# Kernel optimization log

Hardware: AMD Instinct MI355X
Metric: run time of the kernel (lower is better)

Reference implementation:

```python
import jax, jax.numpy as jnp
import numpy as np

ALPHA = 0.2  # LeakyReLU negative slope
NEG_INF = -9e15


def setup_inputs() -> dict:
    key = jax.random.key(0)
    k1, k2, k3, k4 = jax.random.split(key, 4)
    B, C_in, N, L, F_out = 8, 32, 2048, 12, 32
    h = jax.random.normal(k1, (B, C_in, N, L), dtype=jnp.float32)
    adj = jax.random.randint(k2, (N, N), 0, 2, dtype=jnp.int32)
    # xavier_uniform with gain=1.414
    def xavier(k, shape, gain=1.414):
        fan_in, fan_out = shape[0], shape[1]
        bound = gain * np.sqrt(6.0 / (fan_in + fan_out))
        return jax.random.uniform(k, shape, jnp.float32, -bound, bound)
    W = xavier(k3, (C_in, F_out))
    a = xavier(k4, (2 * F_out, 1))
    return {"h": h, "adj": adj, "W": W, "a": a}


def reference(h, adj, W, a):
    # h: (B, C_in, N, L); W: (C_in, F); a: (2F, 1); adj: (N, N)
    B, C_in, N, L = h.shape
    F_out = W.shape[1]
    # Wh: (B, L, N, F)  == torch's (B*L, N, F) reshaped
    Wh = jnp.einsum('bcnl,cf->blnf', h, W)
    # Attention scores use only the last time step (torch slices [:, -1] of e)
    Wh_last = Wh[:, -1]                      # (B, N, F)
    s1 = Wh_last @ a[:F_out, 0]              # (B, N)
    s2 = Wh_last @ a[F_out:, 0]              # (B, N)
    e = s1[:, :, None] + s2[:, None, :]      # (B, N, N)
    e = jnp.where(e > 0, e, ALPHA * e)       # LeakyReLU
    e = jnp.where(adj[None] > 0, e, NEG_INF)
    attn = jax.nn.softmax(e, axis=1)         # softmax over rows (dim=1)
    # dropout skipped (eval mode)
    # h_prime[b,l,w,f] = sum_v Wh[b,l,v,f] * attn[b,v,w]
    h_prime = jnp.einsum('blvf,bvw->blwf', Wh, attn)
    out = jax.nn.elu(h_prime)                # concat=True branch
    return out.transpose(0, 3, 2, 1)         # (B, F, N, L)
```

## Files before the change

kernel.cpp:

```cpp
#include <hip/hip_runtime.h>
#include <hip/hip_bf16.h>
#include <math.h>


constexpr int Cin = 32;
constexpr int Nn  = 2048;
constexpr int Ln  = 12;
constexpr int Fn  = 32;
constexpr int LF  = Ln * Fn;
constexpr int NW  = Nn / 32;
constexpr int CH  = 128;
constexpr int NCH = Nn / CH;
constexpr int WT  = 64;
constexpr int MH  = 192;

typedef short short8 __attribute__((ext_vector_type(8)));
typedef float f32x4  __attribute__((ext_vector_type(4)));

static __device__ __forceinline__ unsigned short f2bf(float x) {
    unsigned u = __builtin_bit_cast(unsigned, x);
    u += 0x7FFFu + ((u >> 16) & 1u);
    return (unsigned short)(u >> 16);
}

__global__ __launch_bounds__(256) void k_adjbits(const int* __restrict__ adj,
                                                 unsigned* __restrict__ bits) {
    int id = blockIdx.x * 256 + threadIdx.x;
    int w  = id & (Nn - 1);
    int vw = id >> 11;
    unsigned m = 0u;
    int base = vw * 32 * Nn + w;
    #pragma unroll
    for (int k = 0; k < 32; ++k)
        m |= (adj[base + k * Nn] > 0 ? 1u : 0u) << k;
    bits[w * NW + vw] = m;
}

__global__ __launch_bounds__(256) void k_wh(const float* __restrict__ h,
                                            const float* __restrict__ W,
                                            const float* __restrict__ a,
                                            unsigned short* __restrict__ WhT,
                                            float* __restrict__ s1,
                                            float* __restrict__ s2,
                                            float* __restrict__ E1,
                                            float* __restrict__ E2) {
    __shared__ float hs[Cin][8][Ln];
    __shared__ float Ws[Cin][Fn];
    int b  = blockIdx.y;
    int n0 = blockIdx.x * 8;
    int tid = threadIdx.x;
    for (int i = tid; i < Cin * Fn; i += 256) Ws[i >> 5][i & 31] = W[i];
    for (int i = tid; i < Cin * 8 * Ln; i += 256) {
        int c = i / (8 * Ln);
        int r = i % (8 * Ln);
        hs[c][r / Ln][r % Ln] = h[(((size_t)b * Cin + c) * Nn + (n0 + r / Ln)) * Ln + (r % Ln)];
    }
    __syncthreads();
    int f  = tid & 31;
    int nl = tid >> 5;
    int n  = n0 + nl;
    float last = 0.f;
    #pragma unroll
    for (int l = 0; l < Ln; ++l) {
        float acc = 0.f;
        #pragma unroll
        for (int c = 0; c < Cin; ++c) acc += hs[c][nl][l] * Ws[c][f];
        WhT[((size_t)b * LF + l * Fn + f) * Nn + n] = f2bf(acc);
        if (l == Ln - 1) last = acc;
    }
    float r1 = last * a[f];
    float r2 = last * a[Fn + f];
    #pragma unroll
    for (int off = 16; off >= 1; off >>= 1) {
        r1 += __shfl_xor(r1, off);
        r2 += __shfl_xor(r2, off);
    }
    if (f == 0) {
        s1[b * Nn + n] = r1;
        s2[b * Nn + n] = r2;
        E1[b * Nn + n] = __expf(r1);
        E2[b * Nn + n] = __expf(0.2f * r1);
    }
}

__global__ __launch_bounds__(256) void k_smax(const float* __restrict__ s1,
                                              float* __restrict__ Mb) {
    int b = blockIdx.x;
    float m = -1e30f;
    for (int i = threadIdx.x; i < Nn; i += 256) m = fmaxf(m, s1[b * Nn + i]);
    #pragma unroll
    for (int off = 32; off >= 1; off >>= 1) m = fmaxf(m, __shfl_xor(m, off));
    __shared__ float wr[4];
    if ((threadIdx.x & 63) == 0) wr[threadIdx.x >> 6] = m;
    __syncthreads();
    if (threadIdx.x == 0)
        Mb[b] = fmaxf(fmaxf(wr[0], wr[1]), fmaxf(wr[2], wr[3]));
}

__global__ __launch_bounds__(256) void k_colinfo(const unsigned* __restrict__ bits,
                                                 int* __restrict__ empty) {
    int w = blockIdx.x * 256 + threadIdx.x;
    const uint4* p = (const uint4*)(bits + (size_t)w * NW);
    unsigned acc = 0;
    #pragma unroll
    for (int i = 0; i < 16; ++i) { uint4 v = p[i]; acc |= v.x | v.y | v.z | v.w; }
    empty[w] = (acc == 0u) ? 1 : 0;
}

__global__ __launch_bounds__(256, 2) void k_gemm(const unsigned short* __restrict__ WhT,
                                                 const float* __restrict__ s2,
                                                 const float* __restrict__ Mb,
                                                 const float* __restrict__ E1,
                                                 const float* __restrict__ E2,
                                                 const unsigned* __restrict__ bits,
                                                 const int* __restrict__ empty,
                                                 float* __restrict__ out) {
    int id = blockIdx.x;
    int b_ = id & 7;
    int r2 = id >> 3;
    int wt = r2 & 31;
    int mh = r2 >> 5;
    int w0 = wt * WT;
    int tid  = threadIdx.x;
    int lane = tid & 63;
    int wv   = tid >> 6;
    int lr   = lane & 15;
    int lg   = lane >> 4;
    int rbase = mh * MH + wv * 48;

    __shared__ unsigned short P[2][WT * CH];
    __shared__ float denom[WT];

    int vgrp = tid & 15;
    int wgrp = tid >> 4;
    int vs   = vgrp * 8;

    const float* E1b = E1 + (size_t)b_ * Nn;
    const float* E2b = E2 + (size_t)b_ * Nn;

    float F1[4], F2[4], G[4], Uv[4];
    float MbV = Mb[b_];
    #pragma unroll
    for (int i = 0; i < 4; ++i) {
        int w = w0 + wgrp * 4 + i;
        float s2w = s2[(size_t)b_ * Nn + w];
        float mz  = MbV + s2w;
        float mw  = fmaxf(mz, 0.2f * mz);
        F1[i] = __expf(s2w - mw);
        F2[i] = __expf(0.2f * s2w - mw);
        G[i]  = __expf(-s2w);
        Uv[i] = empty[w] ? 1.0f : 0.0f;
    }

    if (tid < WT) denom[tid] = 0.f;
    __syncthreads();

    auto gen = [&](int c, int buf) {
        int v0 = c * CH + vs;
        f32x4 e1a = *(const f32x4*)(E1b + v0);
        f32x4 e1b = *(const f32x4*)(E1b + v0 + 4);
        f32x4 e2a = *(const f32x4*)(E2b + v0);
        f32x4 e2b = *(const f32x4*)(E2b + v0 + 4);
        int wi = v0 >> 5;
        int sh = v0 & 31;
        float dsum[4];
        #pragma unroll
        for (int i = 0; i < 4; ++i) {
            int wl = wgrp * 4 + i;
            unsigned bm = (bits[(size_t)(w0 + wl) * NW + wi] >> sh) & 0xffu;
            short8 sv;
            float ds = 0.f;
            #pragma unroll
            for (int j = 0; j < 8; ++j) {
                float e1 = (j < 4) ? e1a[j] : e1b[j - 4];
                float e2 = (j < 4) ? e2a[j] : e2b[j - 4];
                bool pos = e1 > G[i];
                float t = (pos ? e1 : e2) * (pos ? F1[i] : F2[i]);
                float p = ((bm >> j) & 1u) ? t : Uv[i];
                ds += p;
                sv[j] = (short)f2bf(p);
            }
            int idx = (wl * CH + vs) ^ ((wl & 7) << 3);
            *(short8*)&P[buf][idx] = sv;
            dsum[i] = ds;
        }
        #pragma unroll
        for (int off = 1; off < 16; off <<= 1) {
            #pragma unroll
            for (int i = 0; i < 4; ++i) dsum[i] += __shfl_xor(dsum[i], off);
        }
        if (vgrp == 0) {
            #pragma unroll
            for (int i = 0; i < 4; ++i) denom[wgrp * 4 + i] += dsum[i];
        }
    };

    f32x4 acc[3][4];
    #pragma unroll
    for (int r = 0; r < 3; ++r)
        #pragma unroll
        for (int nf = 0; nf < 4; ++nf) acc[r][nf] = (f32x4){0.f, 0.f, 0.f, 0.f};

    const unsigned short* Ab = WhT + (size_t)b_ * LF * Nn;
    const unsigned short* Arow[3];
    #pragma unroll
    for (int r = 0; r < 3; ++r)
        Arow[r] = Ab + (size_t)(rbase + r * 16 + lr) * Nn;

    auto mfma_chunk = [&](int c, int buf) {
        #pragma unroll
        for (int ks = 0; ks < 4; ++ks) {
            int vb = c * CH + ks * 32 + lg * 8;
            short8 af[3];
            #pragma unroll
            for (int r = 0; r < 3; ++r)
                af[r] = *(const short8*)(Arow[r] + vb);
            #pragma unroll
            for (int nf = 0; nf < 4; ++nf) {
                int row = nf * 16 + lr;
                int idx = (row * CH + ks * 32 + lg * 8) ^ ((row & 7) << 3);
                short8 bf = *(const short8*)&P[buf][idx];
                #pragma unroll
                for (int r = 0; r < 3; ++r)
                    acc[r][nf] = __builtin_amdgcn_mfma_f32_16x16x32_bf16(af[r], bf, acc[r][nf], 0, 0, 0);
            }
        }
    };

    gen(0, 0);
    __syncthreads();
    for (int c = 0; c < NCH - 1; ++c) {
        gen(c + 1, (c + 1) & 1);
        mfma_chunk(c, c & 1);
        __syncthreads();
    }
    mfma_chunk(NCH - 1, (NCH - 1) & 1);

    float rdv[4];
    #pragma unroll
    for (int nf = 0; nf < 4; ++nf) rdv[nf] = 1.0f / denom[nf * 16 + lr];

    #pragma unroll
    for (int r = 0; r < 3; ++r)
        #pragma unroll
        for (int nf = 0; nf < 4; ++nf)
            #pragma unroll
            for (int q = 0; q < 4; ++q) {
                int lf = rbase + r * 16 + lg * 4 + q;
                int l = lf >> 5, f = lf & 31;
                float v = acc[r][nf][q] * rdv[nf];
                v = (v > 0.f) ? v : expm1f(v);
                out[(((size_t)b_ * Fn + f) * Nn + (w0 + nf * 16 + lr)) * Ln + l] = v;
            }
}

extern "C" void kernel_launch(void* const* d_in, const int* in_sizes, int n_in,
                              void* d_out, int out_size, void* d_ws, size_t ws_size,
                              hipStream_t stream) {
    (void)in_sizes; (void)n_in; (void)out_size; (void)ws_size;
    const float* h   = (const float*)d_in[0];
    const int*   adj = (const int*)d_in[1];
    const float* W   = (const float*)d_in[2];
    const float* a   = (const float*)d_in[3];
    float* out = (float*)d_out;

    char* ws = (char*)d_ws;
    unsigned short* WhT = (unsigned short*)(ws);
    float*    s1    = (float*)(ws + 12582912);
    float*    s2    = (float*)(ws + 12648448);
    float*    E1    = (float*)(ws + 12713984);
    float*    E2    = (float*)(ws + 12779520);
    float*    Mb    = (float*)(ws + 12845056);
    unsigned* bits  = (unsigned*)(ws + 12845312);
    int*      empty = (int*)(ws + 13369600);

    k_adjbits<<<512, 256, 0, stream>>>(adj, bits);
    k_wh<<<dim3(256, 8), 256, 0, stream>>>(h, W, a, WhT, s1, s2, E1, E2);
    k_smax<<<8, 256, 0, stream>>>(s1, Mb);
    k_colinfo<<<8, 256, 0, stream>>>(bits, empty);
    k_gemm<<<512, 256, 0, stream>>>(WhT, s2, Mb, E1, E2, bits, empty, out);
}
```

Baseline: 223.9 us.

## Restructure GEMM tiling, coalesce Wh and output stores, merge aux kernels

The attention GEMM now gives each block all 384 L·F rows for a 32-column tile, using 512 threads with one column per thread group. Probabilities for that tile are therefore generated once instead of twice across M halves. The epilogue stages accumulators through shared memory so each thread writes 12 contiguous floats with vector stores. k_wh transposes its bf16 results through shared memory for coalesced 16-byte stores and keeps W in registers. The two small reduction kernels are merged into one launch. The trade-offs are more LDS use and extra barriers per block.

```diff
diff --git a/kernel.cpp b/kernel.cpp
--- a/kernel.cpp
+++ b/kernel.cpp
@@ -3,7 +3,6 @@
 #include <math.h>
 
 
-constexpr int Cin = 32;
 constexpr int Nn  = 2048;
 constexpr int Ln  = 12;
 constexpr int Fn  = 32;
@@ -11,8 +10,7 @@
 constexpr int NW  = Nn / 32;
 constexpr int CH  = 128;
 constexpr int NCH = Nn / CH;
-constexpr int WT  = 64;
-constexpr int MH  = 192;
+constexpr int WT  = 32;
 
 typedef short short8 __attribute__((ext_vector_type(8)));
 typedef float f32x4  __attribute__((ext_vector_type(4)));
@@ -44,28 +42,37 @@
                                             float* __restrict__ s2,
                                             float* __restrict__ E1,
                                             float* __restrict__ E2) {
-    __shared__ float hs[Cin][8][Ln];
-    __shared__ float Ws[Cin][Fn];
+    __shared__ float hs[96][33];
+    __shared__ unsigned short T2[8][392];
     int b  = blockIdx.y;
     int n0 = blockIdx.x * 8;
     int tid = threadIdx.x;
-    for (int i = tid; i < Cin * Fn; i += 256) Ws[i >> 5][i & 31] = W[i];
-    for (int i = tid; i < Cin * 8 * Ln; i += 256) {
-        int c = i / (8 * Ln);
-        int r = i % (8 * Ln);
-        hs[c][r / Ln][r % Ln] = h[(((size_t)b * Cin + c) * Nn + (n0 + r / Ln)) * Ln + (r % Ln)];
-    }
-    __syncthreads();
+
+    for (int i = tid; i < 32 * 96; i += 256) {
+        int c = i / 96, r = i % 96;
+        hs[r][c] = h[(size_t)(b * 32 + c) * (Nn * Ln) + n0 * Ln + r];
+    }
     int f  = tid & 31;
     int nl = tid >> 5;
-    int n  = n0 + nl;
+    float Wc[32];
+    #pragma unroll
+    for (int c = 0; c < 32; ++c) Wc[c] = W[c * 32 + f];
+    __syncthreads();
+
     float last = 0.f;
     #pragma unroll
     for (int l = 0; l < Ln; ++l) {
+        const float* hr = &hs[nl * Ln + l][0];
         float acc = 0.f;
         #pragma unroll
-        for (int c = 0; c < Cin; ++c) acc += hs[c][nl][l] * Ws[c][f];
-        WhT[((size_t)b * LF + l * Fn + f) * Nn + n] = f2bf(acc);
+        for (int cq = 0; cq < 8; ++cq) {
+            f32x4 hv = *(const f32x4*)(hr + cq * 4);
+            acc = fmaf(hv[0], Wc[cq * 4 + 0], acc);
+            acc = fmaf(hv[1], Wc[cq * 4 + 1], acc);
+            acc = fmaf(hv[2], Wc[cq * 4 + 2], acc);
+            acc = fmaf(hv[3], Wc[cq * 4 + 3], acc);
+        }
+        T2[nl][l * 32 + f] = f2bf(acc);
         if (l == Ln - 1) last = acc;
     }
     float r1 = last * a[f];
@@ -76,38 +83,49 @@
         r2 += __shfl_xor(r2, off);
     }
     if (f == 0) {
+        int n = n0 + nl;
         s1[b * Nn + n] = r1;
         s2[b * Nn + n] = r2;
         E1[b * Nn + n] = __expf(r1);
         E2[b * Nn + n] = __expf(0.2f * r1);
     }
-}
-
-__global__ __launch_bounds__(256) void k_smax(const float* __restrict__ s1,
-                                              float* __restrict__ Mb) {
-    int b = blockIdx.x;
-    float m = -1e30f;
-    for (int i = threadIdx.x; i < Nn; i += 256) m = fmaxf(m, s1[b * Nn + i]);
-    #pragma unroll
-    for (int off = 32; off >= 1; off >>= 1) m = fmaxf(m, __shfl_xor(m, off));
-    __shared__ float wr[4];
-    if ((threadIdx.x & 63) == 0) wr[threadIdx.x >> 6] = m;
-    __syncthreads();
-    if (threadIdx.x == 0)
-        Mb[b] = fmaxf(fmaxf(wr[0], wr[1]), fmaxf(wr[2], wr[3]));
-}
-
-__global__ __launch_bounds__(256) void k_colinfo(const unsigned* __restrict__ bits,
-                                                 int* __restrict__ empty) {
-    int w = blockIdx.x * 256 + threadIdx.x;
-    const uint4* p = (const uint4*)(bits + (size_t)w * NW);
-    unsigned acc = 0;
-    #pragma unroll
-    for (int i = 0; i < 16; ++i) { uint4 v = p[i]; acc |= v.x | v.y | v.z | v.w; }
-    empty[w] = (acc == 0u) ? 1 : 0;
-}
-
-__global__ __launch_bounds__(256, 2) void k_gemm(const unsigned short* __restrict__ WhT,
+    __syncthreads();
+    for (int r = tid; r < LF; r += 256) {
+        unsigned d0 = (unsigned)T2[0][r] | ((unsigned)T2[1][r] << 16);
+        unsigned d1 = (unsigned)T2[2][r] | ((unsigned)T2[3][r] << 16);
+        unsigned d2 = (unsigned)T2[4][r] | ((unsigned)T2[5][r] << 16);
+        unsigned d3 = (unsigned)T2[6][r] | ((unsigned)T2[7][r] << 16);
+        uint4 val = {d0, d1, d2, d3};
+        *(uint4*)&WhT[((size_t)b * LF + r) * Nn + n0] = val;
+    }
+}
+
+__global__ __launch_bounds__(256) void k_aux(const float* __restrict__ s1,
+                                             const unsigned* __restrict__ bits,
+                                             float* __restrict__ Mb,
+                                             int* __restrict__ empty) {
+    if (blockIdx.x < 8) {
+        int b = blockIdx.x;
+        float m = -1e30f;
+        for (int i = threadIdx.x; i < Nn; i += 256) m = fmaxf(m, s1[b * Nn + i]);
+        #pragma unroll
+        for (int off = 32; off >= 1; off >>= 1) m = fmaxf(m, __shfl_xor(m, off));
+        __shared__ float wr[4];
+        if ((threadIdx.x & 63) == 0) wr[threadIdx.x >> 6] = m;
+        __syncthreads();
+        if (threadIdx.x == 0)
+            Mb[b] = fmaxf(fmaxf(wr[0], wr[1]), fmaxf(wr[2], wr[3]));
+    } else {
+        int w = (blockIdx.x - 8) * 256 + threadIdx.x;
+        const uint4* p = (const uint4*)(bits + (size_t)w * NW);
+        unsigned acc = 0;
+        #pragma unroll
+        for (int i = 0; i < 16; ++i) { uint4 v = p[i]; acc |= v.x | v.y | v.z | v.w; }
+        empty[w] = (acc == 0u) ? 1 : 0;
+    }
+}
+
+__global__ __launch_bounds__(512, 4) void k_gemm(const unsigned short* __restrict__ WhT,
                                                  const float* __restrict__ s2,
                                                  const float* __restrict__ Mb,
                                                  const float* __restrict__ E1,
@@ -117,89 +135,64 @@
                                                  float* __restrict__ out) {
     int id = blockIdx.x;
     int b_ = id & 7;
-    int r2 = id >> 3;
-    int wt = r2 & 31;
-    int mh = r2 >> 5;
+    int wt = id >> 3;
     int w0 = wt * WT;
     int tid  = threadIdx.x;
     int lane = tid & 63;
     int wv   = tid >> 6;
     int lr   = lane & 15;
     int lg   = lane >> 4;
-    int rbase = mh * MH + wv * 48;
+    int rbase = wv * 48;
 
     __shared__ unsigned short P[2][WT * CH];
+    __shared__ float T[LF][17];
     __shared__ float denom[WT];
 
     int vgrp = tid & 15;
-    int wgrp = tid >> 4;
+    int wl   = tid >> 4;
     int vs   = vgrp * 8;
+    int w    = w0 + wl;
 
     const float* E1b = E1 + (size_t)b_ * Nn;
     const float* E2b = E2 + (size_t)b_ * Nn;
-
-    float F1[4], F2[4], G[4], Uv[4];
-    float MbV = Mb[b_];
-    #pragma unroll
-    for (int i = 0; i < 4; ++i) {
-        int w = w0 + wgrp * 4 + i;
-        float s2w = s2[(size_t)b_ * Nn + w];
-        float mz  = MbV + s2w;
-        float mw  = fmaxf(mz, 0.2f * mz);
-        F1[i] = __expf(s2w - mw);
-        F2[i] = __expf(0.2f * s2w - mw);
-        G[i]  = __expf(-s2w);
-        Uv[i] = empty[w] ? 1.0f : 0.0f;
-    }
-
-    if (tid < WT) denom[tid] = 0.f;
-    __syncthreads();
+    const unsigned* bw = bits + (size_t)w * NW;
+
+    float s2w = s2[(size_t)b_ * Nn + w];
+    float mz  = Mb[b_] + s2w;
+    float mw  = fmaxf(mz, 0.2f * mz);
+    float F1  = __expf(s2w - mw);
+    float F2  = __expf(0.2f * s2w - mw);
+    float G   = __expf(-s2w);
+    float Uv  = empty[w] ? 1.0f : 0.0f;
+    float dsum = 0.f;
 
     auto gen = [&](int c, int buf) {
         int v0 = c * CH + vs;
         f32x4 e1a = *(const f32x4*)(E1b + v0);
-        f32x4 e1b = *(const f32x4*)(E1b + v0 + 4);
+        f32x4 e1c = *(const f32x4*)(E1b + v0 + 4);
         f32x4 e2a = *(const f32x4*)(E2b + v0);
-        f32x4 e2b = *(const f32x4*)(E2b + v0 + 4);
-        int wi = v0 >> 5;
-        int sh = v0 & 31;
-        float dsum[4];
-        #pragma unroll
-        for (int i = 0; i < 4; ++i) {
-            int wl = wgrp * 4 + i;
-            unsigned bm = (bits[(size_t)(w0 + wl) * NW + wi] >> sh) & 0xffu;
-            short8 sv;
-            float ds = 0.f;
-            #pragma unroll
-            for (int j = 0; j < 8; ++j) {
-                float e1 = (j < 4) ? e1a[j] : e1b[j - 4];
-                float e2 = (j < 4) ? e2a[j] : e2b[j - 4];
-                bool pos = e1 > G[i];
-                float t = (pos ? e1 : e2) * (pos ? F1[i] : F2[i]);
-                float p = ((bm >> j) & 1u) ? t : Uv[i];
-                ds += p;
-                sv[j] = (short)f2bf(p);
-            }
-            int idx = (wl * CH + vs) ^ ((wl & 7) << 3);
-            *(short8*)&P[buf][idx] = sv;
-            dsum[i] = ds;
-        }
-        #pragma unroll
-        for (int off = 1; off < 16; off <<= 1) {
-            #pragma unroll
-            for (int i = 0; i < 4; ++i) dsum[i] += __shfl_xor(dsum[i], off);
-        }
-        if (vgrp == 0) {
-            #pragma unroll
-            for (int i = 0; i < 4; ++i) denom[wgrp * 4 + i] += dsum[i];
-        }
+        f32x4 e2c = *(const f32x4*)(E2b + v0 + 4);
+        unsigned bm = (bw[v0 >> 5] >> (v0 & 31)) & 0xffu;
+        short8 sv;
+        #pragma unroll
+        for (int j = 0; j < 8; ++j) {
+            float e1 = (j < 4) ? e1a[j] : e1c[j - 4];
+            float e2 = (j < 4) ? e2a[j] : e2c[j - 4];
+            bool pos = e1 > G;
+            float t = (pos ? e1 : e2) * (pos ? F1 : F2);
+            float p = ((bm >> j) & 1u) ? t : Uv;
+            dsum += p;
+            sv[j] = (short)f2bf(p);
+        }
+        int idx = (wl * CH + vs) ^ ((wl & 7) << 3);
+        *(short8*)&P[buf][idx] = sv;
     };
 
-    f32x4 acc[3][4];
+    f32x4 acc[3][2];
     #pragma unroll
     for (int r = 0; r < 3; ++r)
         #pragma unroll
-        for (int nf = 0; nf < 4; ++nf) acc[r][nf] = (f32x4){0.f, 0.f, 0.f, 0.f};
+        for (int nf = 0; nf < 2; ++nf) acc[r][nf] = (f32x4){0.f, 0.f, 0.f, 0.f};
 
     const unsigned short* Ab = WhT + (size_t)b_ * LF * Nn;
     const unsigned short* Arow[3];
@@ -216,7 +209,7 @@
             for (int r = 0; r < 3; ++r)
                 af[r] = *(const short8*)(Arow[r] + vb);
             #pragma unroll
-            for (int nf = 0; nf < 4; ++nf) {
+            for (int nf = 0; nf < 2; ++nf) {
                 int row = nf * 16 + lr;
                 int idx = (row * CH + ks * 32 + lg * 8) ^ ((row & 7) << 3);
                 short8 bf = *(const short8*)&P[buf][idx];
@@ -236,22 +229,36 @@
     }
     mfma_chunk(NCH - 1, (NCH - 1) & 1);
 
-    float rdv[4];
-    #pragma unroll
-    for (int nf = 0; nf < 4; ++nf) rdv[nf] = 1.0f / denom[nf * 16 + lr];
-
-    #pragma unroll
-    for (int r = 0; r < 3; ++r)
-        #pragma unroll
-        for (int nf = 0; nf < 4; ++nf)
-            #pragma unroll
-            for (int q = 0; q < 4; ++q) {
-                int lf = rbase + r * 16 + lg * 4 + q;
-                int l = lf >> 5, f = lf & 31;
-                float v = acc[r][nf][q] * rdv[nf];
-                v = (v > 0.f) ? v : expm1f(v);
-                out[(((size_t)b_ * Fn + f) * Nn + (w0 + nf * 16 + lr)) * Ln + l] = v;
+    #pragma unroll
+    for (int off = 1; off < 16; off <<= 1) dsum += __shfl_xor(dsum, off);
+    if (vgrp == 0) denom[wl] = dsum;
+    __syncthreads();
+
+    int fE  = tid >> 4;
+    int wlE = tid & 15;
+    #pragma unroll
+    for (int nf = 0; nf < 2; ++nf) {
+        #pragma unroll
+        for (int r = 0; r < 3; ++r)
+            #pragma unroll
+            for (int q = 0; q < 4; ++q)
+                T[rbase + r * 16 + lg * 4 + q][lr] = acc[r][nf][q];
+        __syncthreads();
+        {
+            float rdv = 1.0f / denom[nf * 16 + wlE];
+            float vals[12];
+            #pragma unroll
+            for (int l = 0; l < Ln; ++l) {
+                float v = T[l * 32 + fE][wlE] * rdv;
+                vals[l] = (v > 0.f) ? v : expm1f(v);
             }
+            float* ob = out + ((size_t)(b_ * Fn + fE) * Nn + w0 + nf * 16 + wlE) * Ln;
+            *(f32x4*)(ob + 0) = (f32x4){vals[0], vals[1], vals[2], vals[3]};
+            *(f32x4*)(ob + 4) = (f32x4){vals[4], vals[5], vals[6], vals[7]};
+            *(f32x4*)(ob + 8) = (f32x4){vals[8], vals[9], vals[10], vals[11]};
+        }
+        __syncthreads();
+    }
 }
 
 extern "C" void kernel_launch(void* const* d_in, const int* in_sizes, int n_in,
@@ -276,7 +283,6 @@
 
     k_adjbits<<<512, 256, 0, stream>>>(adj, bits);
     k_wh<<<dim3(256, 8), 256, 0, stream>>>(h, W, a, WhT, s1, s2, E1, E2);
-    k_smax<<<8, 256, 0, stream>>>(s1, Mb);
-    k_colinfo<<<8, 256, 0, stream>>>(bits, empty);
-    k_gemm<<<512, 256, 0, stream>>>(WhT, s2, Mb, E1, E2, bits, empty, out);
-}
+    k_aux<<<16, 256, 0, stream>>>(s1, bits, Mb, empty);
+    k_gemm<<<512, 512, 0, stream>>>(WhT, s2, Mb, E1, E2, bits, empty, out);
+}
```

New measurement: 265.5 us. 1.19x slower.
